# Kernel tuning notes

Hardware: AMD Instinct MI355X
Metric: run time of the kernel (lower is better)

The kernel has to match this reference:

```python
import jax, jax.numpy as jnp
import numpy as np


def setup_inputs() -> dict:
    key = jax.random.key(0)
    k1, k2 = jax.random.split(key)
    N, T, C, HW, G = 8, 16, 256, 3136, 8
    x = jax.random.normal(k1, (N, T, C, HW), dtype=jnp.float32)
    # signed temporal shifts in [-4, 3]
    shift = jax.random.randint(k2, (N, G), 0, 8, dtype=jnp.int32) - 4
    return {"x": x, "shift": shift}


def reference(x, shift):
    """Temporal Interlace Shift.

    x:     [N, T, C, HW] feature map
    shift: [N, G] integer temporal shifts, one per channel group (G divides C)
    out[n, t, c, hw] = x[n, t + shift[n, c // (C//G)], c, hw] if the source
    frame index is in [0, T), else 0 (matches the CUDA kernel which writes
    into a zero-initialized output and skips out-of-range source frames).
    """
    N, T, C, HW = x.shape
    G = shift.shape[1]
    gc = C // G  # channels per shift group
    ch_shift = jnp.repeat(shift, gc, axis=1)  # [N, C]
    t_src = jnp.arange(T, dtype=jnp.int32)[None, :, None] + ch_shift[:, None, :]  # [N, T, C]
    valid = (t_src >= 0) & (t_src < T)  # [N, T, C]
    idx = jnp.clip(t_src, 0, T - 1)[..., None]  # [N, T, C, 1], broadcasts over HW
    out = jnp.take_along_axis(x, idx, axis=1)  # [N, T, C, HW]
    return jnp.where(valid[..., None], out, jnp.zeros((), x.dtype))
```

## Files before the change

### kernel.cpp

```cpp
#include <hip/hip_runtime.h>


typedef float f32x4 __attribute__((ext_vector_type(4)));

#define TIN_N   8
#define TIN_T   16
#define TIN_C   256
#define TIN_G   8
#define TIN_HW4 784
#define T_STRIDE4 (TIN_C * TIN_HW4)
#define BLK_ELEMS (TIN_T * TIN_HW4)
#define BLK_ITERS (BLK_ELEMS / 256)

__global__ __launch_bounds__(256) void tin_shift_kernel(
    const f32x4* __restrict__ x4,
    const int*   __restrict__ shift,
    f32x4*       __restrict__ out4)
{
    const int nc = blockIdx.x;
    const int c  = nc & (TIN_C - 1);
    const int n  = nc >> 8;
    const int s  = shift[n * TIN_G + (c >> 5)];

    const size_t base = ((size_t)n * (TIN_T * TIN_C) + c) * TIN_HW4;
    const long   soff = (long)s * T_STRIDE4;

    const int tid = threadIdx.x;

    #pragma unroll 7
    for (int it = 0; it < BLK_ITERS; ++it) {
        const int f  = it * 256 + tid;
        const int t  = f / TIN_HW4;
        const int hw = f - t * TIN_HW4;
        const size_t di = base + (size_t)t * T_STRIDE4 + (size_t)hw;

        f32x4 v = (f32x4){0.f, 0.f, 0.f, 0.f};
        if ((unsigned)(t + s) < TIN_T) {
            v = x4[(long)di + soff];
        }
        out4[di] = v;
    }
}

extern "C" void kernel_launch(void* const* d_in, const int* in_sizes, int n_in,
                              void* d_out, int out_size, void* d_ws, size_t ws_size,
                              hipStream_t stream)
{
    const f32x4* x4    = (const f32x4*)d_in[0];
    const int*   shift = (const int*)d_in[1];
    f32x4*       out4  = (f32x4*)d_out;

    tin_shift_kernel<<<TIN_N * TIN_C, 256, 0, stream>>>(x4, shift, out4);
}
```

Measured before the change: 158.6 us.

## Launch one block per (n,t,c) row with block-uniform branch and nontemporal copies

The grid goes from one block per (n,c) looping over all T frames to one block per (n,t,c) row of HW, sixteen times as many blocks. The validity test becomes block-uniform, so out-of-range rows only write zeros and never issue loads. The per-element divide and modulo by HW4 are gone, and loads and stores use nontemporal hints to avoid polluting caches on a pure streaming copy. The cost is more, shorter blocks: each thread does about three iterations with a ragged tail, so launch and scheduling overhead per byte rises.

```diff
diff --git a/kernel.cpp b/kernel.cpp
--- a/kernel.cpp
+++ b/kernel.cpp
@@ -8,37 +8,35 @@
 #define TIN_C   256
 #define TIN_G   8
 #define TIN_HW4 784
-#define T_STRIDE4 (TIN_C * TIN_HW4)
-#define BLK_ELEMS (TIN_T * TIN_HW4)
-#define BLK_ITERS (BLK_ELEMS / 256)
 
 __global__ __launch_bounds__(256) void tin_shift_kernel(
     const f32x4* __restrict__ x4,
     const int*   __restrict__ shift,
     f32x4*       __restrict__ out4)
 {
-    const int nc = blockIdx.x;
-    const int c  = nc & (TIN_C - 1);
-    const int n  = nc >> 8;
+    const int row = blockIdx.x;
+    const int c   = row & (TIN_C - 1);
+    const int t   = (row >> 8) & (TIN_T - 1);
+    const int n   = row >> 12;
+
     const int s  = shift[n * TIN_G + (c >> 5)];
+    const int ts = t + s;
 
-    const size_t base = ((size_t)n * (TIN_T * TIN_C) + c) * TIN_HW4;
-    const long   soff = (long)s * T_STRIDE4;
-
+    f32x4* dst = out4 + (size_t)row * TIN_HW4;
     const int tid = threadIdx.x;
 
-    #pragma unroll 7
-    for (int it = 0; it < BLK_ITERS; ++it) {
-        const int f  = it * 256 + tid;
-        const int t  = f / TIN_HW4;
-        const int hw = f - t * TIN_HW4;
-        const size_t di = base + (size_t)t * T_STRIDE4 + (size_t)hw;
-
-        f32x4 v = (f32x4){0.f, 0.f, 0.f, 0.f};
-        if ((unsigned)(t + s) < TIN_T) {
-            v = x4[(long)di + soff];
+    if ((unsigned)ts < TIN_T) {
+        const f32x4* src = x4 + ((size_t)row + (long)s * TIN_C) * TIN_HW4;
+        #pragma unroll
+        for (int i = tid; i < TIN_HW4; i += 256) {
+            __builtin_nontemporal_store(__builtin_nontemporal_load(&src[i]), &dst[i]);
         }
-        out4[di] = v;
+    } else {
+        const f32x4 z = (f32x4){0.f, 0.f, 0.f, 0.f};
+        #pragma unroll
+        for (int i = tid; i < TIN_HW4; i += 256) {
+            __builtin_nontemporal_store(z, &dst[i]);
+        }
     }
 }
 
@@ -50,5 +48,6 @@
     const int*   shift = (const int*)d_in[1];
     f32x4*       out4  = (f32x4*)d_out;
 
-    tin_shift_kernel<<<TIN_N * TIN_C, 256, 0, stream>>>(x4, shift, out4);
+    const int rows = TIN_N * TIN_T * TIN_C;
+    tin_shift_kernel<<<rows, 256, 0, stream>>>(x4, shift, out4);
 }
```

Measured after the change: 129.9 us. 18.1% less time.
